# Optimization experiments

Hardware: AMD Instinct MI355X
Metric: run time of the kernel (lower is better)

Reference implementation:

```python
import jax, jax.numpy as jnp
import numpy as np


def _conv(x, w, b):
    # PyTorch Conv2d(k=4, s=2, p=1): NCHW x OIHW correlation
    y = jax.lax.conv_general_dilated(x, w, window_strides=(2, 2),
                                     padding=((1, 1), (1, 1)),
                                     dimension_numbers=('NCHW', 'OIHW', 'NCHW'))
    return y + b[None, :, None, None]


def _conv_t(x, w, b):
    # PyTorch ConvTranspose2d(k=4, s=2, p=1); w has torch shape (Cin, Cout, 4, 4).
    # Adjoint of strided correlation = correlation with spatially-flipped,
    # channel-swapped kernel and lhs dilation; pad = k - 1 - p = 2.
    wk = jnp.flip(w, (2, 3)).transpose(1, 0, 2, 3)  # (Cout, Cin, 4, 4)
    y = jax.lax.conv_general_dilated(x, wk, window_strides=(1, 1),
                                     padding=((2, 2), (2, 2)),
                                     lhs_dilation=(2, 2),
                                     dimension_numbers=('NCHW', 'OIHW', 'NCHW'))
    return y + b[None, :, None, None]


def setup_inputs() -> dict:
    key = jax.random.key(0)
    ks = jax.random.split(key, 18)
    s = 0.05
    inp = {'x': jax.random.normal(ks[0], (32, 3, 256, 256), jnp.float32)}
    # encoder weights (OIHW)
    enc_shapes = [(64, 3, 4, 4), (128, 64, 4, 4), (256, 128, 4, 4), (512, 256, 4, 4)]
    for i, sh in enumerate(enc_shapes):
        inp[f'e_w{i+1}'] = jax.random.normal(ks[1 + i], sh, jnp.float32) * s
        inp[f'e_b{i+1}'] = jnp.zeros((sh[0],), jnp.float32)
    # decoder weights (torch ConvTranspose2d layout: Cin, Cout, kH, kW)
    dec_shapes = [(512, 128, 4, 4), (128, 64, 4, 4), (64, 32, 4, 4), (32, 3, 4, 4)]
    for i, sh in enumerate(dec_shapes):
        inp[f'd_w{i+1}'] = jax.random.normal(ks[5 + i], sh, jnp.float32) * s
        inp[f'd_b{i+1}'] = jnp.zeros((sh[1],), jnp.float32)
    # codebook (num_embeddings=1024, embedding_dim=512)
    inp['embed'] = jax.random.normal(ks[9], (1024, 512), jnp.float32)
    return inp


def reference(x, e_w1, e_b1, e_w2, e_b2, e_w3, e_b3, e_w4, e_b4,
              d_w1, d_b1, d_w2, d_b2, d_w3, d_b3, d_w4, d_b4, embed):
    # encoder
    h = jax.nn.relu(_conv(x, e_w1, e_b1))
    h = jax.nn.relu(_conv(h, e_w2, e_b2))
    h = jax.nn.relu(_conv(h, e_w3, e_b3))
    z = jax.nn.relu(_conv(h, e_w4, e_b4))  # (B, 512, 16, 16)
    # quantizer: NCHW -> NHWC -> flat (B*H*W, D)
    B, D, H, W = z.shape
    z_flat = z.transpose(0, 2, 3, 1).reshape(-1, D)
    # squared L2 distance to each code: ||z||^2 - 2 z.E^T + ||E||^2
    dist = (jnp.sum(z_flat ** 2, axis=1, keepdims=True)
            - 2.0 * z_flat @ embed.T
            + jnp.sum(embed ** 2, axis=1))  # (N, K)
    idx = jnp.argmin(dist, axis=1)
    quantized = embed[idx]  # gather == one_hot @ embed
    z_q = quantized.reshape(B, H, W, D).transpose(0, 3, 1, 2)  # NCHW
    # decoder
    h = jax.nn.relu(_conv_t(z_q, d_w1, d_b1))
    h = jax.nn.relu(_conv_t(h, d_w2, d_b2))
    h = jax.nn.relu(_conv_t(h, d_w3, d_b3))
    out = jnp.tanh(_conv_t(h, d_w4, d_b4))  # (B, 3, 256, 256)
    return out
```

## Files before the change

### kernel.cpp

```cpp
#include <hip/hip_runtime.h>
#include <math.h>


typedef __attribute__((ext_vector_type(8))) short bf16x8;
typedef __attribute__((ext_vector_type(4))) float f32x4;
union FragU { unsigned u[4]; bf16x8 v; };

__device__ __forceinline__ unsigned bf16_rne(unsigned u) {
    return (u + 0x7FFFu + ((u >> 16) & 1u)) >> 16;
}
__device__ __forceinline__ unsigned pack_split(float v) {
    unsigned u = __builtin_bit_cast(unsigned, v);
    unsigned hi = bf16_rne(u);
    float hif = __builtin_bit_cast(float, hi << 16);
    float r = v - hif;
    unsigned lo = bf16_rne(__builtin_bit_cast(unsigned, r));
    return hi | (lo << 16);
}

__global__ void __launch_bounds__(256) pack_tensor(
    const float* __restrict__ s, unsigned* __restrict__ d, int n)
{
    int i = blockIdx.x * 256 + threadIdx.x;
    if (i < n) d[i] = pack_split(s[i]);
}

__global__ void __launch_bounds__(256) pack_w1(
    const float* __restrict__ w, unsigned* __restrict__ wq)
{
    int idx = blockIdx.x * 256 + threadIdx.x;
    if (idx >= 64 * 64) return;
    int k = idx & 63, oc = idx >> 6;
    float v = (k < 48) ? w[oc * 48 + k] : 0.0f;
    wq[idx] = pack_split(v);
}

template<int Cout, int K>
__global__ void __launch_bounds__(256) pack_w_planes(
    const float* __restrict__ w, unsigned* __restrict__ wq)
{
    constexpr int K2 = K / 2;
    constexpr int TOT = Cout * K;
    int idx = blockIdx.x * 256 + threadIdx.x;
    if (idx >= TOT) return;
    int kp   = idx % K2;
    int rest = idx / K2;
    int oc   = rest % Cout;
    int p    = rest / Cout;
    unsigned u0 = pack_split(w[(size_t)oc * K + 2 * kp]);
    unsigned u1 = pack_split(w[(size_t)oc * K + 2 * kp + 1]);
    wq[idx] = (p == 0) ? ((u0 & 0xffffu) | (u1 << 16))
                       : ((u0 >> 16) | (u1 & 0xffff0000u));
}

template<int Cin, int Cout>
__global__ void __launch_bounds__(256) repack_wt_planes(
    const float* __restrict__ w, unsigned* __restrict__ wq)
{
    constexpr int K = Cin * 4, K2 = K / 2;
    constexpr int TOT = 2 * 4 * Cout * K2;
    int idx = blockIdx.x * 256 + threadIdx.x;
    if (idx >= TOT) return;
    int kp   = idx % K2;
    int rest = idx / K2;
    int co   = rest % Cout;
    rest    /= Cout;
    int par  = rest & 3;
    int p    = rest >> 2;
    int dy = par >> 1, dx = par & 1;
    unsigned u01[2];
#pragma unroll
    for (int e = 0; e < 2; ++e) {
        int k = 2 * kp + e;
        int t = k & 3, ci = k >> 2;
        int r = t >> 1, s = t & 1;
        int ky = 3 - dy - 2 * r;
        int kx = 3 - dx - 2 * s;
        u01[e] = pack_split(w[(((size_t)ci * Cout + co) * 4 + ky) * 4 + kx]);
    }
    wq[idx] = (p == 0) ? ((u01[0] & 0xffffu) | (u01[1] << 16))
                       : ((u01[0] >> 16) | (u01[1] & 0xffff0000u));
}

__global__ void __launch_bounds__(256) embed_transpose(
    const float* __restrict__ embed, float* __restrict__ et)
{
    int idx = blockIdx.x * 256 + threadIdx.x;
    int c = idx & 1023, k = idx >> 10;
    et[idx] = embed[(size_t)c * 512 + k];
}

template<int Cin, int H, int W, int Cout, int NB, int PACKO>
__global__ void __launch_bounds__(256) conv4s2_mfma(
    const unsigned* __restrict__ xp, const unsigned* __restrict__ wp,
    const float* __restrict__ bias, float* __restrict__ y)
{
    constexpr int OH = H / 2, OW = W / 2;
    constexpr int LOG_OW = (OW == 64) ? 6 : (OW == 32) ? 5 : 4;
    constexpr int R   = 64 / OW;
    constexpr int RT  = 2 * R + 2;
    constexpr int CS  = W + 2;
    constexpr int XEL = 2 * RT * CS;
    constexpr int XIT = (XEL + 255) / 256;
    constexpr int K   = Cin * 16;
    constexpr int K2  = K / 2;
    constexpr int NC  = Cin / 2;
    constexpr int NT  = NB / 64;
    constexpr int WR  = NB / 16;
    constexpr int WIT = NB / 8;
    constexpr int MBC = 32 * OH * OW / 64;
    constexpr int XPAD = (XEL + 7) & ~7;
    constexpr int OFF_WH = XPAD;
    constexpr int OFF_WL = OFF_WH + NB * 20;
    constexpr int OFF_AH = OFF_WL + NB * 20;
    constexpr int OFF_AL = OFF_AH + 64 * 20;
    constexpr int SM1 = OFF_AL + 64 * 20;
    constexpr int SM2 = NB * 68;
    constexpr int SMEM = SM1 > SM2 ? SM1 : SM2;

    __shared__ unsigned smem[SMEM];
    unsigned* raw = smem;
    unsigned* wbh = smem + OFF_WH;
    unsigned* wbl = smem + OFF_WL;
    unsigned* afh = smem + OFF_AH;
    unsigned* afl = smem + OFF_AL;

    int bid = blockIdx.x;
    int mb = bid % MBC, ng = bid / MBC;
    int oc0 = ng * NB;
    int m0 = mb * 64;
    int nimg = m0 / (OH * OW);
    int sp0 = m0 % (OH * OW);
    int oyb = sp0 >> LOG_OW;

    int tid  = threadIdx.x;
    int lane = tid & 63, wv = tid >> 6;
    int lm = lane & 15, q = lane >> 4;
    int n0w = wv * 16 * NT;

    const unsigned* xbase = xp + (size_t)nimg * Cin * H * W;

    int  goff[XIT];
    bool gok[XIT];
#pragma unroll
    for (int s = 0; s < XIT; ++s) {
        int i = tid + 256 * s;
        goff[s] = 0; gok[s] = false;
        if (i < XEL) {
            int lc = i % CS;
            int t2 = i / CS;
            int lr = t2 % RT;
            int c  = t2 / RT;
            int gr = 2 * oyb - 1 + lr;
            int gc = lc - 1;
            bool ok = ((unsigned)gr < (unsigned)H) && ((unsigned)gc < (unsigned)W);
            goff[s] = ok ? (c * H * W + gr * W + gc) : 0;
            gok[s]  = ok;
        }
    }
    const unsigned* wbase_h = wp + (size_t)(oc0 + (tid >> 4)) * K2 + (tid & 15);
    const unsigned* wbase_l = wbase_h + (size_t)Cout * K2;
    int wlds0 = (tid >> 4) * 20 + (tid & 15);

    f32x4 acc[4][NT];
#pragma unroll
    for (int nt = 0; nt < NT; ++nt) {
        float b = bias[oc0 + n0w + nt * 16 + lm];
#pragma unroll
        for (int mt = 0; mt < 4; ++mt)
#pragma unroll
            for (int r = 0; r < 4; ++r) acc[mt][nt][r] = b;
    }

    unsigned pfa[XIT];
    unsigned pfb[WIT];

    auto load_chunk = [&](int ch) {
        const unsigned* cb = xbase + (size_t)(ch * 2) * (H * W);
#pragma unroll
        for (int s = 0; s < XIT; ++s) {
            unsigned v = 0;
            if (gok[s]) v = cb[goff[s]];
            pfa[s] = v;
        }
        const unsigned* wch = wbase_h + ch * 16;
        const unsigned* wcl = wbase_l + ch * 16;
#pragma unroll
        for (int s = 0; s < WR; ++s) {
            pfb[2 * s]     = wch[(size_t)s * 16 * K2];
            pfb[2 * s + 1] = wcl[(size_t)s * 16 * K2];
        }
    };
    auto store_chunk = [&]() {
#pragma unroll
        for (int s = 0; s < XIT; ++s) {
            int i = tid + 256 * s;
            if (i < XEL) raw[i] = pfa[s];
        }
#pragma unroll
        for (int s = 0; s < WR; ++s) {
            wbh[wlds0 + s * 16 * 20] = pfb[2 * s];
            wbl[wlds0 + s * 16 * 20] = pfb[2 * s + 1];
        }
    };

    load_chunk(0);
#pragma unroll 1
    for (int ch = 0; ch < NC; ++ch) {
        __syncthreads();
        store_chunk();
        __syncthreads();
        {
            int m = tid >> 2, blk = tid & 3;
            int oyl = m >> LOG_OW, oxl = m & (OW - 1);
            unsigned h[4], l[4];
#pragma unroll
            for (int j = 0; j < 4; ++j) {
                int kp = blk * 4 + j;
                int c = kp >> 3, ky = (kp >> 1) & 3, kxp = kp & 1;
                int ro = (c * RT + 2 * oyl + ky) * CS + 2 * oxl + 2 * kxp;
                unsigned r0 = raw[ro], r1 = raw[ro + 1];
                h[j] = (r0 & 0xffffu) | (r1 << 16);
                l[j] = (r0 >> 16) | (r1 & 0xffff0000u);
            }
            uint4 vh; vh.x = h[0]; vh.y = h[1]; vh.z = h[2]; vh.w = h[3];
            uint4 vl; vl.x = l[0]; vl.y = l[1]; vl.z = l[2]; vl.w = l[3];
            *(uint4*)&afh[m * 20 + blk * 4] = vh;
            *(uint4*)&afl[m * 20 + blk * 4] = vl;
        }
        if (ch + 1 < NC) load_chunk(ch + 1);
        __syncthreads();

        FragU bhi[NT], blo[NT];
#pragma unroll
        for (int nt = 0; nt < NT; ++nt) {
            int oc = n0w + nt * 16 + lm;
            uint4 th = *(const uint4*)&wbh[oc * 20 + q * 4];
            uint4 tl = *(const uint4*)&wbl[oc * 20 + q * 4];
            bhi[nt].u[0] = th.x; bhi[nt].u[1] = th.y;
            bhi[nt].u[2] = th.z; bhi[nt].u[3] = th.w;
            blo[nt].u[0] = tl.x; blo[nt].u[1] = tl.y;
            blo[nt].u[2] = tl.z; blo[nt].u[3] = tl.w;
        }
#pragma unroll
        for (int mt = 0; mt < 4; ++mt) {
            int m = mt * 16 + lm;
            uint4 ah = *(const uint4*)&afh[m * 20 + q * 4];
            uint4 al = *(const uint4*)&afl[m * 20 + q * 4];
            FragU ahi, alo;
            ahi.u[0] = ah.x; ahi.u[1] = ah.y; ahi.u[2] = ah.z; ahi.u[3] = ah.w;
            alo.u[0] = al.x; alo.u[1] = al.y; alo.u[2] = al.z; alo.u[3] = al.w;
#pragma unroll
            for (int nt = 0; nt < NT; ++nt) {
                acc[mt][nt] = __builtin_amdgcn_mfma_f32_16x16x32_bf16(
                    ahi.v, bhi[nt].v, acc[mt][nt], 0, 0, 0);
                acc[mt][nt] = __builtin_amdgcn_mfma_f32_16x16x32_bf16(
                    ahi.v, blo[nt].v, acc[mt][nt], 0, 0, 0);
                acc[mt][nt] = __builtin_amdgcn_mfma_f32_16x16x32_bf16(
                    alo.v, bhi[nt].v, acc[mt][nt], 0, 0, 0);
            }
        }
    }

    __syncthreads();
    float* cs = (float*)smem;
#pragma unroll
    for (int mt = 0; mt < 4; ++mt)
#pragma unroll
        for (int nt = 0; nt < NT; ++nt) {
            int nl = n0w + nt * 16 + lm;
#pragma unroll
            for (int r = 0; r < 4; ++r)
                cs[nl * 68 + mt * 16 + q * 4 + r] = acc[mt][nt][r];
        }
    __syncthreads();
    {
        constexpr int QT = 256 / NB;
        constexpr int MQ = 64 / QT;
        int nl = tid / QT, qt = tid % QT;
        size_t gb = ((size_t)(nimg * Cout + oc0 + nl)) * (OH * OW) + sp0 + qt * MQ;
#pragma unroll
        for (int i2 = 0; i2 < MQ / 4; ++i2) {
            float4 v = *(float4*)&cs[nl * 68 + qt * MQ + 4 * i2];
            v.x = fmaxf(v.x, 0.0f); v.y = fmaxf(v.y, 0.0f);
            v.z = fmaxf(v.z, 0.0f); v.w = fmaxf(v.w, 0.0f);
            if (PACKO) {
                uint4 p;
                p.x = pack_split(v.x); p.y = pack_split(v.y);
                p.z = pack_split(v.z); p.w = pack_split(v.w);
                *(uint4*)((unsigned*)y + gb + 4 * i2) = p;
            } else {
                *(float4*)(y + gb + 4 * i2) = v;
            }
        }
    }
}

template<int Cin, int CINR, int H, int W, int Cout, int MT, int NT, int PACKO>
__global__ void __launch_bounds__(256) conv4s2_mfma_g(
    const unsigned* __restrict__ xp, const unsigned* __restrict__ wp,
    const float* __restrict__ bias, float* __restrict__ y)
{
    constexpr int OH = H / 2, OW = W / 2;
    constexpr int OWB = (OW >= 64) ? 64 : OW;
    constexpr int LOG_OWB = (OWB == 64) ? 6 : (OWB == 32) ? 5 : 4;
    constexpr int LOG_OW  = (OW == 128) ? 7 : (OW == 64) ? 6 : (OW == 32) ? 5 : 4;
    constexpr int R   = 64 / OWB;
    constexpr int RT  = 2 * R + 2;
    constexpr int CS  = 2 * OWB + 2;
    constexpr int XEL = 2 * RT * CS;
    constexpr int XIT = (XEL + 255) / 256;
    constexpr int K   = Cin * 16;
    constexpr int NC  = Cin / 2;
    constexpr int NB  = Cout;
    constexpr int WIT = NB / 8;
    constexpr int WN  = Cout / (16 * NT);
    constexpr int WM  = 4 / WN;
    static_assert(WM * MT * 16 == 64, "M tiling");
    static_assert(WN * NT * 16 == Cout, "N tiling");
    constexpr int MBC = 32 * OH * OW / 64;
    constexpr int XPAD = (XEL + 7) & ~7;
    constexpr int SM1 = XPAD + NB * 36;
    constexpr int SM2 = NB * 68;
    constexpr int SMEM = SM1 > SM2 ? SM1 : SM2;

    __shared__ unsigned smem[SMEM];
    unsigned* raw = smem;
    unsigned* wb  = smem + XPAD;

    int bid = blockIdx.x;
    int mb = bid % MBC, ng = bid / MBC;
    int oc0 = ng * NB;
    int m0 = mb * 64;
    int nimg = m0 / (OH * OW);
    int sp0 = m0 % (OH * OW);
    int oyb = sp0 >> LOG_OW;
    int oxb = sp0 & (OW - 1);

    int tid  = threadIdx.x;
    int lane = tid & 63, wv = tid >> 6;
    int lm = lane & 15, q = lane >> 4;
    int wm = wv / WN, wn = wv % WN;

    const unsigned* xbase = xp + (size_t)nimg * CINR * H * W;

    int  goff[XIT];
    bool gok[XIT];
    int  cidx[XIT];
#pragma unroll
    for (int s = 0; s < XIT; ++s) {
        int i = tid + 256 * s;
        goff[s] = 0; gok[s] = false; cidx[s] = 0;
        if (i < XEL) {
            int lc = i % CS;
            int t2 = i / CS;
            int lr = t2 % RT;
            int c  = t2 / RT;
            int gr = 2 * oyb - 1 + lr;
            int gc = 2 * oxb - 1 + lc;
            bool ok = ((unsigned)gr < (unsigned)H) && ((unsigned)gc < (unsigned)W);
            goff[s] = ok ? (c * H * W + gr * W + gc) : 0;
            gok[s]  = ok;
            cidx[s] = c;
        }
    }
    const unsigned* wbase = wp + (size_t)(oc0 + (tid >> 5)) * K + (tid & 31);
    int wlds0 = (tid >> 5) * 36 + (tid & 31);

    f32x4 acc[MT][NT];
#pragma unroll
    for (int nt = 0; nt < NT; ++nt) {
        float b = bias[oc0 + wn * NT * 16 + nt * 16 + lm];
#pragma unroll
        for (int mt = 0; mt < MT; ++mt)
#pragma unroll
            for (int r = 0; r < 4; ++r) acc[mt][nt][r] = b;
    }

    unsigned pfa[XIT];
    unsigned pfb[WIT];

    auto load_chunk = [&](int ch) {
        const unsigned* cb = xbase + (size_t)(ch * 2) * (H * W);
#pragma unroll
        for (int s = 0; s < XIT; ++s) {
            unsigned v = 0;
            bool okc = (2 * ch + cidx[s]) < CINR;
            if (gok[s] && okc) v = cb[goff[s]];
            pfa[s] = v;
        }
        const unsigned* wc = wbase + ch * 32;
#pragma unroll
        for (int s = 0; s < WIT; ++s) pfb[s] = wc[(size_t)s * 8 * K];
    };
    auto store_chunk = [&]() {
#pragma unroll
        for (int s = 0; s < XIT; ++s) {
            int i = tid + 256 * s;
            if (i < XEL) raw[i] = pfa[s];
        }
#pragma unroll
        for (int s = 0; s < WIT; ++s) wb[wlds0 + s * 288] = pfb[s];
    };

    load_chunk(0);
#pragma unroll 1
    for (int ch = 0; ch < NC; ++ch) {
        __syncthreads();
        store_chunk();
        __syncthreads();
        if (ch + 1 < NC) load_chunk(ch + 1);

        FragU bhi[NT], blo[NT];
#pragma unroll
        for (int nt = 0; nt < NT; ++nt) {
            const unsigned* bp = &wb[(wn * NT * 16 + nt * 16 + lm) * 36 + q * 8];
            uint4 p0 = *(const uint4*)bp;
            uint4 p1 = *(const uint4*)(bp + 4);
            unsigned e0 = p0.x, e1 = p0.y, e2 = p0.z, e3 = p0.w;
            unsigned e4 = p1.x, e5 = p1.y, e6 = p1.z, e7 = p1.w;
            bhi[nt].u[0] = (e0 & 0xffffu) | (e1 << 16);
            bhi[nt].u[1] = (e2 & 0xffffu) | (e3 << 16);
            bhi[nt].u[2] = (e4 & 0xffffu) | (e5 << 16);
            bhi[nt].u[3] = (e6 & 0xffffu) | (e7 << 16);
            blo[nt].u[0] = (e0 >> 16) | (e1 & 0xffff0000u);
            blo[nt].u[1] = (e2 >> 16) | (e3 & 0xffff0000u);
            blo[nt].u[2] = (e4 >> 16) | (e5 & 0xffff0000u);
            blo[nt].u[3] = (e6 >> 16) | (e7 & 0xffff0000u);
        }
#pragma unroll
        for (int mt = 0; mt < MT; ++mt) {
            int m = wm * (MT * 16) + mt * 16 + lm;
            int oyl = m >> LOG_OWB, oxl = m & (OWB - 1);
            int c = q >> 1, rb = 2 * oyl + (q & 1) * 2;
            const unsigned* rp = &raw[(c * RT + rb) * CS + 2 * oxl];
            uint2 a0 = *(const uint2*)rp;
            uint2 a1 = *(const uint2*)(rp + 2);
            uint2 a2 = *(const uint2*)(rp + CS);
            uint2 a3 = *(const uint2*)(rp + CS + 2);
            FragU ahi, alo;
            ahi.u[0] = (a0.x & 0xffffu) | (a0.y << 16);
            ahi.u[1] = (a1.x & 0xffffu) | (a1.y << 16);
            ahi.u[2] = (a2.x & 0xffffu) | (a2.y << 16);
            ahi.u[3] = (a3.x & 0xffffu) | (a3.y << 16);
            alo.u[0] = (a0.x >> 16) | (a0.y & 0xffff0000u);
            alo.u[1] = (a1.x >> 16) | (a1.y & 0xffff0000u);
            alo.u[2] = (a2.x >> 16) | (a2.y & 0xffff0000u);
            alo.u[3] = (a3.x >> 16) | (a3.y & 0xffff0000u);
#pragma unroll
            for (int nt = 0; nt < NT; ++nt) {
                acc[mt][nt] = __builtin_amdgcn_mfma_f32_16x16x32_bf16(
                    ahi.v, bhi[nt].v, acc[mt][nt], 0, 0, 0);
                acc[mt][nt] = __builtin_amdgcn_mfma_f32_16x16x32_bf16(
                    ahi.v, blo[nt].v, acc[mt][nt], 0, 0, 0);
                acc[mt][nt] = __builtin_amdgcn_mfma_f32_16x16x32_bf16(
                    alo.v, bhi[nt].v, acc[mt][nt], 0, 0, 0);
            }
        }
    }

    __syncthreads();
    float* cs = (float*)smem;
#pragma unroll
    for (int mt = 0; mt < MT; ++mt)
#pragma unroll
        for (int nt = 0; nt < NT; ++nt) {
            int nl  = wn * NT * 16 + nt * 16 + lm;
            int mb2 = wm * (MT * 16) + mt * 16 + q * 4;
#pragma unroll
            for (int r = 0; r < 4; ++r)
                cs[nl * 68 + mb2 + r] = acc[mt][nt][r];
        }
    __syncthreads();
    {
        constexpr int QT = 256 / NB;
        constexpr int MQ = 64 / QT;
        int nl = tid / QT, qt = tid % QT;
        size_t gb = ((size_t)(nimg * Cout + oc0 + nl)) * (OH * OW) + sp0 + qt * MQ;
#pragma unroll
        for (int i2 = 0; i2 < MQ / 4; ++i2) {
            float4 v = *(float4*)&cs[nl * 68 + qt * MQ + 4 * i2];
            v.x = fmaxf(v.x, 0.0f); v.y = fmaxf(v.y, 0.0f);
            v.z = fmaxf(v.z, 0.0f); v.w = fmaxf(v.w, 0.0f);
            if (PACKO) {
                uint4 p;
                p.x = pack_split(v.x); p.y = pack_split(v.y);
                p.z = pack_split(v.z); p.w = pack_split(v.w);
                *(uint4*)((unsigned*)y + gb + 4 * i2) = p;
            } else {
                *(float4*)(y + gb + 4 * i2) = v;
            }
        }
    }
}

template<int Cin, int Hh, int Wh, int Cout, int MT, int NT, int PACKO>
__global__ void __launch_bounds__(256) convt4s2_mfma(
    const unsigned* __restrict__ xp, const unsigned* __restrict__ wq,
    const float* __restrict__ bias, float* __restrict__ y)
{
    constexpr int W = Wh;
    constexpr int LOG_W = (W == 64) ? 6 : (W == 32) ? 5 : 4;
    constexpr int R   = 64 / W;
    constexpr int RT  = R + 1;
    constexpr int CS  = W + 2;
    constexpr int XEL = 8 * RT * CS;
    constexpr int XIT = (XEL + 255) / 256;
    constexpr int K   = Cin * 4;
    constexpr int K2  = K / 2;
    constexpr int NC  = Cin / 8;
    constexpr int NB  = Cout;
    constexpr int WR  = NB / 16;
    constexpr int WIT = NB / 8;
    constexpr int WN  = Cout / (16 * NT);
    constexpr int WM  = 4 / WN;
    static_assert(WM * MT * 16 == 64, "M tiling");
    static_assert(WN * NT * 16 == Cout, "N tiling");
    constexpr int MBC = 32 * Hh * W / 64;
    constexpr int XPAD = (XEL + 7) & ~7;
    constexpr int OFF_WH = XPAD;
    constexpr int OFF_WL = OFF_WH + NB * 20;
    constexpr int OFF_AH = OFF_WL + NB * 20;
    constexpr int OFF_AL = OFF_AH + 64 * 20;
    constexpr int SM1 = OFF_AL + 64 * 20;
    constexpr int SM2 = NB * 68;
    constexpr int SMEM = SM1 > SM2 ? SM1 : SM2;

    __shared__ unsigned smem[SMEM];
    unsigned* raw = smem;
    unsigned* wbh = smem + OFF_WH;
    unsigned* wbl = smem + OFF_WL;
    unsigned* afh = smem + OFF_AH;
    unsigned* afl = smem + OFF_AL;

    int bid = blockIdx.x;
    int mb  = bid % MBC;
    int par = bid / MBC;
    int dy = par >> 1, dx = par & 1;

    int m0   = mb * 64;
    int nimg = m0 / (Hh * W);
    int sp0  = m0 % (Hh * W);
    int il0  = sp0 >> LOG_W;

    int tid = threadIdx.x;
    int lane = tid & 63, wv = tid >> 6;
    int lm = lane & 15, q = lane >> 4;
    int wm = wv / WN, wn = wv % WN;

    const unsigned* xbase = xp + (size_t)nimg * Cin * Hh * W;

    int  goff[XIT];
    bool gok[XIT];
#pragma unroll
    for (int s = 0; s < XIT; ++s) {
        int i = tid + 256 * s;
        goff[s] = 0; gok[s] = false;
        if (i < XEL) {
            int lc = i % CS;
            int t2 = i / CS;
            int lr = t2 % RT;
            int c  = t2 / RT;
            int gr = il0 - 1 + dy + lr;
            int gc = lc - 1;
            bool ok = ((unsigned)gr < (unsigned)Hh) && ((unsigned)gc < (unsigned)W);
            goff[s] = ok ? (c * Hh * W + gr * W + gc) : 0;
            gok[s]  = ok;
        }
    }
    const unsigned* wbase_h = wq + (size_t)(par * Cout + (tid >> 4)) * K2 + (tid & 15);
    const unsigned* wbase_l = wbase_h + (size_t)4 * Cout * K2;
    int wlds0 = (tid >> 4) * 20 + (tid & 15);

    f32x4 acc[MT][NT];
#pragma unroll
    for (int nt = 0; nt < NT; ++nt) {
        float b = bias[wn * NT * 16 + nt * 16 + lm];
#pragma unroll
        for (int mt = 0; mt < MT; ++mt)
#pragma unroll
            for (int r = 0; r < 4; ++r) acc[mt][nt][r] = b;
    }

    unsigned pfa[XIT];
    unsigned pfb[WIT];

    auto load_chunk = [&](int ch) {
        const unsigned* cb = xbase + (size_t)(ch * 8) * (Hh * W);
#pragma unroll
        for (int s = 0; s < XIT; ++s) {
            unsigned v = 0;
            if (gok[s]) v = cb[goff[s]];
            pfa[s] = v;
        }
        const unsigned* wch = wbase_h + ch * 16;
        const unsigned* wcl = wbase_l + ch * 16;
#pragma unroll
        for (int s = 0; s < WR; ++s) {
            pfb[2 * s]     = wch[(size_t)s * 16 * K2];
            pfb[2 * s + 1] = wcl[(size_t)s * 16 * K2];
        }
    };
    auto store_chunk = [&]() {
#pragma unroll
        for (int s = 0; s < XIT; ++s) {
            int i = tid + 256 * s;
            if (i < XEL) raw[i] = pfa[s];
        }
#pragma unroll
        for (int s = 0; s < WR; ++s) {
            wbh[wlds0 + s * 16 * 20] = pfb[2 * s];
            wbl[wlds0 + s * 16 * 20] = pfb[2 * s + 1];
        }
    };

    load_chunk(0);
#pragma unroll 1
    for (int ch = 0; ch < NC; ++ch) {
        __syncthreads();
        store_chunk();
        __syncthreads();
        {
            int m = tid >> 2, blk = tid & 3;
            int il = m >> LOG_W, jl = m & (W - 1);
            unsigned h[4], l[4];
#pragma unroll
            for (int j = 0; j < 4; ++j) {
                int kp = blk * 4 + j;
                int cl = kp >> 1, r = kp & 1;
                int ro = (cl * RT + il + r) * CS + jl + dx;
                unsigned r0 = raw[ro], r1 = raw[ro + 1];
                h[j] = (r0 & 0xffffu) | (r1 << 16);
                l[j] = (r0 >> 16) | (r1 & 0xffff0000u);
            }
            uint4 vh; vh.x = h[0]; vh.y = h[1]; vh.z = h[2]; vh.w = h[3];
            uint4 vl; vl.x = l[0]; vl.y = l[1]; vl.z = l[2]; vl.w = l[3];
            *(uint4*)&afh[m * 20 + blk * 4] = vh;
            *(uint4*)&afl[m * 20 + blk * 4] = vl;
        }
        if (ch + 1 < NC) load_chunk(ch + 1);
        __syncthreads();

        FragU bhi[NT], blo[NT];
#pragma unroll
        for (int nt = 0; nt < NT; ++nt) {
            int oc = wn * NT * 16 + nt * 16 + lm;
            uint4 th = *(const uint4*)&wbh[oc * 20 + q * 4];
            uint4 tl = *(const uint4*)&wbl[oc * 20 + q * 4];
            bhi[nt].u[0] = th.x; bhi[nt].u[1] = th.y;
            bhi[nt].u[2] = th.z; bhi[nt].u[3] = th.w;
            blo[nt].u[0] = tl.x; blo[nt].u[1] = tl.y;
            blo[nt].u[2] = tl.z; blo[nt].u[3] = tl.w;
        }
#pragma unroll
        for (int mt = 0; mt < MT; ++mt) {
            int ml = wm * (MT * 16) + mt * 16 + lm;
            uint4 ah = *(const uint4*)&afh[ml * 20 + q * 4];
            uint4 al = *(const uint4*)&afl[ml * 20 + q * 4];
            FragU ahi, alo;
            ahi.u[0] = ah.x; ahi.u[1] = ah.y; ahi.u[2] = ah.z; ahi.u[3] = ah.w;
            alo.u[0] = al.x; alo.u[1] = al.y; alo.u[2] = al.z; alo.u[3] = al.w;
#pragma unroll
            for (int nt = 0; nt < NT; ++nt) {
                acc[mt][nt] = __builtin_amdgcn_mfma_f32_16x16x32_bf16(
                    ahi.v, bhi[nt].v, acc[mt][nt], 0, 0, 0);
                acc[mt][nt] = __builtin_amdgcn_mfma_f32_16x16x32_bf16(
                    ahi.v, blo[nt].v, acc[mt][nt], 0, 0, 0);
                acc[mt][nt] = __builtin_amdgcn_mfma_f32_16x16x32_bf16(
                    alo.v, bhi[nt].v, acc[mt][nt], 0, 0, 0);
            }
        }
    }

    __syncthreads();
    float* cs = (float*)smem;
#pragma unroll
    for (int mt = 0; mt < MT; ++mt)
#pragma unroll
        for (int nt = 0; nt < NT; ++nt) {
            int nl  = wn * NT * 16 + nt * 16 + lm;
            int mb2 = wm * (MT * 16) + mt * 16 + q * 4;
#pragma unroll
            for (int r = 0; r < 4; ++r)
                cs[nl * 68 + mb2 + r] = acc[mt][nt][r];
        }
    __syncthreads();
    constexpr int EIT = NB * 64 / 256;
#pragma unroll
    for (int it = 0; it < EIT; ++it) {
        int idx = tid + 256 * it;
        int c = idx >> 6, m = idx & 63;
        int il = m >> LOG_W, jl = m & (W - 1);
        int oy = 2 * (il0 + il) + dy;
        int ox = 2 * jl + dx;
        float v = fmaxf(cs[c * 68 + m], 0.0f);
        size_t go = (((size_t)(nimg * Cout + c)) * (2 * Hh) + oy) * (2 * W) + ox;
        if (PACKO) ((unsigned*)y)[go] = pack_split(v);
        else       y[go] = v;
    }
}

template<int Cin, int H, int W, int Cout, int COT, int ACT, int UNR>
__global__ void __launch_bounds__(256) convt4s2_k(
    const float* __restrict__ x, const float* __restrict__ w,
    const float* __restrict__ bias, float* __restrict__ y)
{
    constexpr int OH = 2 * H, OW = 2 * W, OWq = OW / 4;
    int id = blockIdx.x * 256 + threadIdx.x;
    int ox4 = id % OWq; int t = id / OWq;
    int oy  = t % OH;   t /= OH;
    int cog = t % (Cout / COT);
    int n   = t / (Cout / COT);
    int co0 = __builtin_amdgcn_readfirstlane(cog * COT);
    n       = __builtin_amdgcn_readfirstlane(n);

    int p   = (oy + 1) & 1;
    int iyA = (oy + 1 - p) >> 1;
    int iyB = iyA - 1;
    bool vA = (iyA < H);
    bool vB = (iyB >= 0);
    int iyAc = vA ? iyA : 0, iyBc = vB ? iyB : 0;

    int t0 = 2 * ox4;
    bool c0 = (t0 - 1 >= 0);
    bool c3 = (t0 + 2 <= W - 1);
    int j0 = c0 ? t0 - 1 : 0;
    int j3 = c3 ? t0 + 2 : 0;

    float acc[COT][4];
#pragma unroll
    for (int o = 0; o < COT; ++o) {
        float b = bias[co0 + o];
#pragma unroll
        for (int j = 0; j < 4; ++j) acc[o][j] = b;
    }

    const float* xn = x + (size_t)n * Cin * H * W;

#pragma unroll UNR
    for (int ci = 0; ci < Cin; ++ci) {
        const float* xc  = xn + (size_t)ci * (H * W);
        const float* xrA = xc + (size_t)iyAc * W;
        const float* xrB = xc + (size_t)iyBc * W;
        float a0 = (vA && c0) ? xrA[j0]     : 0.0f;
        float a1 =  vA        ? xrA[t0]     : 0.0f;
        float a2 =  vA        ? xrA[t0 + 1] : 0.0f;
        float a3 = (vA && c3) ? xrA[j3]     : 0.0f;
        float b0 = (vB && c0) ? xrB[j0]     : 0.0f;
        float b1 =  vB        ? xrB[t0]     : 0.0f;
        float b2 =  vB        ? xrB[t0 + 1] : 0.0f;
        float b3 = (vB && c3) ? xrB[j3]     : 0.0f;

        const float* wci = w + ((size_t)ci * Cout + co0) * 16;
#pragma unroll
        for (int o = 0; o < COT; ++o) {
            const float* wr = wci + (size_t)o * 16;
            float wA0 = wr[p * 4 + 0], wA1 = wr[p * 4 + 1];
            float wA2 = wr[p * 4 + 2], wA3 = wr[p * 4 + 3];
            float wB0 = wr[(p + 2) * 4 + 0], wB1 = wr[(p + 2) * 4 + 1];
            float wB2 = wr[(p + 2) * 4 + 2], wB3 = wr[(p + 2) * 4 + 3];
            acc[o][0] = fmaf(a1, wA1, acc[o][0]); acc[o][0] = fmaf(a0, wA3, acc[o][0]);
            acc[o][0] = fmaf(b1, wB1, acc[o][0]); acc[o][0] = fmaf(b0, wB3, acc[o][0]);
            acc[o][1] = fmaf(a2, wA0, acc[o][1]); acc[o][1] = fmaf(a1, wA2, acc[o][1]);
            acc[o][1] = fmaf(b2, wB0, acc[o][1]); acc[o][1] = fmaf(b1, wB2, acc[o][1]);
            acc[o][2] = fmaf(a2, wA1, acc[o][2]); acc[o][2] = fmaf(a1, wA3, acc[o][2]);
            acc[o][2] = fmaf(b2, wB1, acc[o][2]); acc[o][2] = fmaf(b1, wB3, acc[o][2]);
            acc[o][3] = fmaf(a3, wA0, acc[o][3]); acc[o][3] = fmaf(a2, wA2, acc[o][3]);
            acc[o][3] = fmaf(b3, wB0, acc[o][3]); acc[o][3] = fmaf(b2, wB2, acc[o][3]);
        }
    }

    int ox0 = ox4 * 4;
#pragma unroll
    for (int o = 0; o < COT; ++o) {
        float* yr = y + (((size_t)n * Cout + co0 + o) * OH + oy) * OW + ox0;
#pragma unroll
        for (int j = 0; j < 4; ++j) {
            float v = acc[o][j];
            yr[j] = (ACT == 0) ? fmaxf(v, 0.0f) : tanhf(v);
        }
    }
}

__global__ void __launch_bounds__(256) embed_norms(
    const float* __restrict__ embed, float* __restrict__ norms)
{
    int c = blockIdx.x * 256 + threadIdx.x;
    const float* e = embed + (size_t)c * 512;
    float s = 0.0f;
    for (int k = 0; k < 512; ++k) s = fmaf(e[k], e[k], s);
    norms[c] = s;
}

__global__ void __launch_bounds__(256, 4) vq_argmin8v(
    const float* __restrict__ z, const float* __restrict__ et,
    const float* __restrict__ norms, int* __restrict__ out)
{
    constexpr int ZS = 516;
    int row0 = blockIdx.x * 8;
    int n    = row0 >> 8;
    int yx0  = row0 & 255;
    int tid  = threadIdx.x;

    __shared__ float zr[8 * ZS];

    const float* zn = z + ((size_t)n * 512) * 256;
#pragma unroll
    for (int it = 0; it < 4; ++it) {
        int i  = tid + 256 * it;
        int rq = i & 1, kc = i >> 1;
        float4 v = *(const float4*)&zn[(size_t)kc * 256 + yx0 + 4 * rq];
        zr[(4 * rq + 0) * ZS + kc] = v.x;
        zr[(4 * rq + 1) * ZS + kc] = v.y;
        zr[(4 * rq + 2) * ZS + kc] = v.z;
        zr[(4 * rq + 3) * ZS + kc] = v.w;
    }
    __syncthreads();

    f32x4 acc[8];
#pragma unroll
    for (int r = 0; r < 8; ++r) acc[r] = (f32x4){0.f, 0.f, 0.f, 0.f};

    const float* ebase = et + 4 * tid;
    f32x4 ev[4], fv[4];
#pragma unroll
    for (int j = 0; j < 4; ++j)
        ev[j] = *(const f32x4*)&ebase[(size_t)j * 1024];

#pragma unroll 1
    for (int k4 = 0; k4 < 128; ++k4) {
        int kn = (k4 + 1 < 128) ? k4 + 1 : 127;
#pragma unroll
        for (int j = 0; j < 4; ++j)
            fv[j] = *(const f32x4*)&ebase[(size_t)(4 * kn + j) * 1024];
#pragma unroll
        for (int r = 0; r < 8; ++r) {
            float4 zz = *(const float4*)&zr[r * ZS + 4 * k4];
            f32x4 a = acc[r];
            a += ev[0] * zz.x;
            a += ev[1] * zz.y;
            a += ev[2] * zz.z;
            a += ev[3] * zz.w;
            acc[r] = a;
        }
#pragma unroll
        for (int j = 0; j < 4; ++j) ev[j] = fv[j];
    }

    float4 nb = *(const float4*)&norms[4 * tid];
    float best[8]; int bi[8];
#pragma unroll
    for (int r = 0; r < 8; ++r) {
        float d0 = nb.x - 2.0f * acc[r][0];
        float d1 = nb.y - 2.0f * acc[r][1];
        float d2 = nb.z - 2.0f * acc[r][2];
        float d3 = nb.w - 2.0f * acc[r][3];
        float b = d0; int ix = 4 * tid;
        if (d1 < b) { b = d1; ix = 4 * tid + 1; }
        if (d2 < b) { b = d2; ix = 4 * tid + 2; }
        if (d3 < b) { b = d3; ix = 4 * tid + 3; }
        best[r] = b; bi[r] = ix;
    }

    __syncthreads();
    float* rbd = zr;
    int*   rbi = (int*)(zr + 2048);
#pragma unroll
    for (int r = 0; r < 8; ++r) {
        rbd[r * 256 + tid] = best[r];
        rbi[r * 256 + tid] = bi[r];
    }
    __syncthreads();
    for (int s = 128; s > 0; s >>= 1) {
        if (tid < s) {
#pragma unroll
            for (int r = 0; r < 8; ++r) {
                int i0 = r * 256 + tid;
                float od = rbd[i0 + s]; int oi = rbi[i0 + s];
                float md = rbd[i0];     int mi = rbi[i0];
                if (od < md || (od == md && oi < mi)) { rbd[i0] = od; rbi[i0] = oi; }
            }
        }
        __syncthreads();
    }
    if (tid < 8) out[row0 + tid] = rbi[tid * 256];
}

__global__ void __launch_bounds__(256) vq_gather_pack(
    const int* __restrict__ vidx, const float* __restrict__ embed,
    unsigned* __restrict__ zq)
{
    int i = blockIdx.x * 256 + threadIdx.x;
    int yx = i & 255;
    int t  = i >> 8;
    int c  = t & 511;
    int n  = t >> 9;
    int row = (n << 8) + yx;
    zq[i] = pack_split(embed[(size_t)vidx[row] * 512 + c]);
}

extern "C" void kernel_launch(void* const* d_in, const int* in_sizes, int n_in,
                              void* d_out, int out_size, void* d_ws, size_t ws_size,
                              hipStream_t stream)
{
    (void)in_sizes; (void)n_in; (void)out_size; (void)ws_size;
    const float* x     = (const float*)d_in[0];
    const float* ew1   = (const float*)d_in[1];
    const float* eb1   = (const float*)d_in[2];
    const float* ew2   = (const float*)d_in[3];
    const float* eb2   = (const float*)d_in[4];
    const float* ew3   = (const float*)d_in[5];
    const float* eb3   = (const float*)d_in[6];
    const float* ew4   = (const float*)d_in[7];
    const float* eb4   = (const float*)d_in[8];
    const float* dw1   = (const float*)d_in[9];
    const float* db1   = (const float*)d_in[10];
    const float* dw2   = (const float*)d_in[11];
    const float* db2   = (const float*)d_in[12];
    const float* dw3   = (const float*)d_in[13];
    const float* db3   = (const float*)d_in[14];
    const float* dw4   = (const float*)d_in[15];
    const float* db4   = (const float*)d_in[16];
    const float* embed = (const float*)d_in[17];
    float* out = (float*)d_out;

    unsigned* W0   = (unsigned*)d_ws;
    unsigned* h1p  = W0;
    unsigned* h2p  = W0 + 33554432;
    unsigned* xp1  = W0 + 33554432;
    unsigned* h3p  = W0;
    float*    z    = (float*)(W0 + 8388608);
    unsigned* zq   = W0 + 12582912;
    float*    P0   = (float*)(W0 + 16777216);
    float*    P1   = (float*)(W0 + 20971520);
    int*      vidx = (int*)(W0 + 29360128);
    float*    norms= (float*)(W0 + 29368320);
    float*    g3o  = (float*)h2p;

    unsigned* wp2 = (unsigned*)d_out;
    unsigned* wp3 = wp2 + 131072;
    unsigned* wp4 = wp2 + 655360;
    unsigned* wq1 = wp2 + 2752512;
    unsigned* wq2 = wq1 + 1048576;
    unsigned* wq3 = wq2 + 131072;
    float*    et  = (float*)(wq3 + 32768);
    unsigned* wp1 = (unsigned*)(et + 524288);

    dim3 b256(256);

    pack_w_planes<128, 1024><<<dim3(512),  b256, 0, stream>>>(ew2, wp2);
    pack_w_planes<256, 2048><<<dim3(2048), b256, 0, stream>>>(ew3, wp3);
    pack_w_planes<512, 4096><<<dim3(8192), b256, 0, stream>>>(ew4, wp4);
    pack_w1<<<dim3(16), b256, 0, stream>>>(ew1, wp1);
    pack_tensor<<<dim3(24576), b256, 0, stream>>>(x, xp1, 6291456);
    repack_wt_planes<512, 128><<<dim3(4096), b256, 0, stream>>>(dw1, wq1);
    repack_wt_planes<128,  64><<<dim3(512),  b256, 0, stream>>>(dw2, wq2);
    repack_wt_planes< 64,  32><<<dim3(128),  b256, 0, stream>>>(dw3, wq3);
    embed_transpose<<<dim3(2048), b256, 0, stream>>>(embed, et);

    conv4s2_mfma_g<4, 3, 256, 256, 64, 4, 1, 1><<<dim3(8192), b256, 0, stream>>>(
        xp1, wp1, eb1, (float*)h1p);
    conv4s2_mfma<64, 128, 128, 128, 128, 1><<<dim3(2048), b256, 0, stream>>>(
        h1p, wp2, eb2, (float*)h2p);
    conv4s2_mfma<128, 64, 64, 256, 128, 1><<<dim3(1024), b256, 0, stream>>>(
        h2p, wp3, eb3, (float*)h3p);
    conv4s2_mfma<256, 32, 32, 512, 64, 0><<<dim3(1024), b256, 0, stream>>>(
        h3p, wp4, eb4, z);

    embed_norms<<<dim3(4), b256, 0, stream>>>(embed, norms);
    vq_argmin8v<<<dim3(1024), b256, 0, stream>>>(z, et, norms, vidx);
    vq_gather_pack<<<dim3(16384), b256, 0, stream>>>(vidx, embed, zq);

    convt4s2_mfma<512, 16, 16, 128, 4, 2, 1><<<dim3(4 * 128), b256, 0, stream>>>(
        zq, wq1, db1, P0);
    convt4s2_mfma<128, 32, 32, 64, 4, 1, 1><<<dim3(4 * 512), b256, 0, stream>>>(
        (const unsigned*)P0, wq2, db2, P1);
    convt4s2_mfma<64, 64, 64, 32, 2, 1, 0><<<dim3(4 * 2048), b256, 0, stream>>>(
        (const unsigned*)P1, wq3, db3, g3o);
    convt4s2_k<32, 128, 128, 3, 3, 1, 2><<<dim3(2048), b256, 0, stream>>>(
        g3o, dw4, db4, out);
}
```

Before: 1.149 ms.

## Split raw input tile into hi/lo bf16 planes and read MFMA fragments directly

The encoder conv kernel now stores the staged input tile as two separate 16-bit planes (hi and lo bf16 parts) with a padded row stride. The A fragments are read straight from those planes, which removes the intermediate im2col repack into afh/afl, its shared memory, and one __syncthreads per chunk. In exchange the stores become 16-bit, and the fragment reads are four 32-bit loads per plane, which may be unaligned or cause bank conflicts.

```diff
diff --git a/kernel.cpp b/kernel.cpp
--- a/kernel.cpp
+++ b/kernel.cpp
@@ -100,6 +100,7 @@
     constexpr int R   = 64 / OW;
     constexpr int RT  = 2 * R + 2;
     constexpr int CS  = W + 2;
+    constexpr int CS2 = CS + 2;
     constexpr int XEL = 2 * RT * CS;
     constexpr int XIT = (XEL + 255) / 256;
     constexpr int K   = Cin * 16;
@@ -109,21 +110,19 @@
     constexpr int WR  = NB / 16;
     constexpr int WIT = NB / 8;
     constexpr int MBC = 32 * OH * OW / 64;
-    constexpr int XPAD = (XEL + 7) & ~7;
-    constexpr int OFF_WH = XPAD;
+    constexpr int RAWU = RT * CS2;
+    constexpr int OFF_RL = RAWU;
+    constexpr int OFF_WH = ((2 * RAWU) + 7) & ~7;
     constexpr int OFF_WL = OFF_WH + NB * 20;
-    constexpr int OFF_AH = OFF_WL + NB * 20;
-    constexpr int OFF_AL = OFF_AH + 64 * 20;
-    constexpr int SM1 = OFF_AL + 64 * 20;
+    constexpr int SM1 = OFF_WL + NB * 20;
     constexpr int SM2 = NB * 68;
     constexpr int SMEM = SM1 > SM2 ? SM1 : SM2;
 
     __shared__ unsigned smem[SMEM];
-    unsigned* raw = smem;
+    unsigned short* rawh = (unsigned short*)smem;
+    unsigned short* rawl = (unsigned short*)(smem + OFF_RL);
     unsigned* wbh = smem + OFF_WH;
     unsigned* wbl = smem + OFF_WL;
-    unsigned* afh = smem + OFF_AH;
-    unsigned* afl = smem + OFF_AL;
 
     int bid = blockIdx.x;
     int mb = bid % MBC, ng = bid / MBC;
@@ -142,10 +141,11 @@
 
     int  goff[XIT];
     bool gok[XIT];
+    int  sidx[XIT];
 #pragma unroll
     for (int s = 0; s < XIT; ++s) {
         int i = tid + 256 * s;
-        goff[s] = 0; gok[s] = false;
+        goff[s] = 0; gok[s] = false; sidx[s] = 0;
         if (i < XEL) {
             int lc = i % CS;
             int t2 = i / CS;
@@ -156,6 +156,7 @@
             bool ok = ((unsigned)gr < (unsigned)H) && ((unsigned)gc < (unsigned)W);
             goff[s] = ok ? (c * H * W + gr * W + gc) : 0;
             gok[s]  = ok;
+            sidx[s] = (c * RT + lr) * CS2 + lc;
         }
     }
     const unsigned* wbase_h = wp + (size_t)(oc0 + (tid >> 4)) * K2 + (tid & 15);
@@ -195,7 +196,10 @@
 #pragma unroll
         for (int s = 0; s < XIT; ++s) {
             int i = tid + 256 * s;
-            if (i < XEL) raw[i] = pfa[s];
+            if (i < XEL) {
+                rawh[sidx[s]] = (unsigned short)(pfa[s] & 0xffffu);
+                rawl[sidx[s]] = (unsigned short)(pfa[s] >> 16);
+            }
         }
 #pragma unroll
         for (int s = 0; s < WR; ++s) {
@@ -210,26 +214,7 @@
         __syncthreads();
         store_chunk();
         __syncthreads();
-        {
-            int m = tid >> 2, blk = tid & 3;
-            int oyl = m >> LOG_OW, oxl = m & (OW - 1);
-            unsigned h[4], l[4];
-#pragma unroll
-            for (int j = 0; j < 4; ++j) {
-                int kp = blk * 4 + j;
-                int c = kp >> 3, ky = (kp >> 1) & 3, kxp = kp & 1;
-                int ro = (c * RT + 2 * oyl + ky) * CS + 2 * oxl + 2 * kxp;
-                unsigned r0 = raw[ro], r1 = raw[ro + 1];
-                h[j] = (r0 & 0xffffu) | (r1 << 16);
-                l[j] = (r0 >> 16) | (r1 & 0xffff0000u);
-            }
-            uint4 vh; vh.x = h[0]; vh.y = h[1]; vh.z = h[2]; vh.w = h[3];
-            uint4 vl; vl.x = l[0]; vl.y = l[1]; vl.z = l[2]; vl.w = l[3];
-            *(uint4*)&afh[m * 20 + blk * 4] = vh;
-            *(uint4*)&afl[m * 20 + blk * 4] = vl;
-        }
         if (ch + 1 < NC) load_chunk(ch + 1);
-        __syncthreads();
 
         FragU bhi[NT], blo[NT];
 #pragma unroll
@@ -245,11 +230,18 @@
 #pragma unroll
         for (int mt = 0; mt < 4; ++mt) {
             int m = mt * 16 + lm;
-            uint4 ah = *(const uint4*)&afh[m * 20 + q * 4];
-            uint4 al = *(const uint4*)&afl[m * 20 + q * 4];
+            int oyl = m >> LOG_OW, oxl = m & (OW - 1);
+            int c = q >> 1, rb = 2 * oyl + (q & 1) * 2;
+            int bidx = (c * RT + rb) * CS2 + 2 * oxl;
             FragU ahi, alo;
-            ahi.u[0] = ah.x; ahi.u[1] = ah.y; ahi.u[2] = ah.z; ahi.u[3] = ah.w;
-            alo.u[0] = al.x; alo.u[1] = al.y; alo.u[2] = al.z; alo.u[3] = al.w;
+            ahi.u[0] = *(const unsigned*)&rawh[bidx];
+            ahi.u[1] = *(const unsigned*)&rawh[bidx + 2];
+            ahi.u[2] = *(const unsigned*)&rawh[bidx + CS2];
+            ahi.u[3] = *(const unsigned*)&rawh[bidx + CS2 + 2];
+            alo.u[0] = *(const unsigned*)&rawl[bidx];
+            alo.u[1] = *(const unsigned*)&rawl[bidx + 2];
+            alo.u[2] = *(const unsigned*)&rawl[bidx + CS2];
+            alo.u[3] = *(const unsigned*)&rawl[bidx + CS2 + 2];
 #pragma unroll
             for (int nt = 0; nt < NT; ++nt) {
                 acc[mt][nt] = __builtin_amdgcn_mfma_f32_16x16x32_bf16(
```

Result: no change. 1.130 ms (-1.6%).
